# Optimization experiments

Measured on AMD Instinct MI355X. Metric: run time of the kernel, lower is better.

Reference implementation:

```python
import jax, jax.numpy as jnp
import numpy as np

B, S, H = 64, 512, 768
N_SPANS, MAX_SPAN, CW = 4, 8, 3
NH = 8
HD = H // NH
W = MAX_SPAN + 1 + 2 * CW  # max context window length (15)
H2 = H // 2
N_ATE, N_SENT = 2, 2


def _ln(x, g, b, eps=1e-5):
    m = x.mean(-1, keepdims=True)
    v = ((x - m) ** 2).mean(-1, keepdims=True)
    return (x - m) / jnp.sqrt(v + eps) * g + b


def _classifier(x, w1, b1, g, bb, w2, b2):
    # Dropout -> Linear -> GELU -> LayerNorm -> Linear (eval mode: dropout = id)
    h = jax.nn.gelu(x @ w1.T + b1, approximate=False)
    h = _ln(h, g, bb)
    return h @ w2.T + b2


def setup_inputs() -> dict:
    key = jax.random.key(0)
    ks = jax.random.split(key, 16)
    p = lambda k, shape: (0.02 * jax.random.normal(k, shape)).astype(jnp.float32)
    seq_out = jax.random.normal(ks[0], (B, S, H), dtype=jnp.float32)
    starts = jax.random.randint(ks[1], (B, N_SPANS), 1, S - MAX_SPAN - 1)
    lens = jax.random.randint(ks[2], (B, N_SPANS), 1, MAX_SPAN + 1)
    ends = starts + lens  # exclusive end, span length in [1, MAX_SPAN]
    return dict(
        seq_out=seq_out,
        span_starts=starts.astype(jnp.int32),
        span_ends=ends.astype(jnp.int32),
        ate_g=jnp.ones((H,), jnp.float32), ate_b=jnp.zeros((H,), jnp.float32),
        apc_g=jnp.ones((H,), jnp.float32), apc_b=jnp.zeros((H,), jnp.float32),
        w_in=p(ks[3], (3 * H, H)), b_in=jnp.zeros((3 * H,), jnp.float32),
        w_out=p(ks[4], (H, H)), b_out=jnp.zeros((H,), jnp.float32),
        fus_w=p(ks[5], (H, 2 * H)), fus_b=jnp.zeros((H,), jnp.float32),
        asp_w1=p(ks[6], (H2, H)), asp_b1=jnp.zeros((H2,), jnp.float32),
        asp_lng=jnp.ones((H2,), jnp.float32), asp_lnb=jnp.zeros((H2,), jnp.float32),
        asp_w2=p(ks[7], (N_ATE, H2)), asp_b2=jnp.zeros((N_ATE,), jnp.float32),
        sen_w1=p(ks[8], (H2, H)), sen_b1=jnp.zeros((H2,), jnp.float32),
        sen_lng=jnp.ones((H2,), jnp.float32), sen_lnb=jnp.zeros((H2,), jnp.float32),
        sen_w2=p(ks[9], (N_SENT, H2)), sen_b2=jnp.zeros((N_SENT,), jnp.float32),
    )


def _fwd(seq_out, ate_g, ate_b, apc_g, apc_b, w_in, b_in, w_out, b_out,
         fus_w, fus_b, asp_w1, asp_b1, asp_lng, asp_lnb, asp_w2, asp_b2,
         sen_w1, sen_b1, sen_lng, sen_lnb, sen_w2, sen_b2,
         span_starts, span_ends):
    dt = seq_out.dtype
    # clamping semantics as in the torch loop
    s = jnp.clip(span_starts, 0, S - 1)
    e = jnp.maximum(s, jnp.minimum(span_ends, S - 1))
    left = jnp.maximum(0, s - CW)
    right = jnp.minimum(S, e + 1 + CW)

    # ATE head over all tokens
    ate_logits = _classifier(_ln(seq_out, ate_g, ate_b),
                             asp_w1, asp_b1, asp_lng, asp_lnb, asp_w2, asp_b2)

    gather = jax.vmap(lambda so, idx: so[idx])  # ([S,H],[N,W]) -> [N,W,H]

    # aspect mean over tokens [s, e)
    aidx = s[..., None] + jnp.arange(MAX_SPAN)          # [B,N,MS]
    va = (aidx < e[..., None]).astype(dt)
    asp_tok = gather(seq_out, jnp.clip(aidx, 0, S - 1)) # [B,N,MS,H]
    cnt = va.sum(-1, keepdims=True)                     # [B,N,1]
    asp_mean = (asp_tok * va[..., None]).sum(-2) / jnp.maximum(cnt, 1.0)
    asp_mean = jnp.where(cnt > 0, asp_mean, seq_out[:, None, 0, :])

    # context window [left, right): tiny self-attention, then mean
    cidx = left[..., None] + jnp.arange(W)              # [B,N,W]
    vc = (cidx < right[..., None]).astype(dt)
    ctx = gather(seq_out, jnp.clip(cidx, 0, S - 1))     # [B,N,W,H]
    qkv = ctx @ w_in.T + b_in
    q, k, v = jnp.split(qkv, 3, axis=-1)
    q = q.reshape(B, N_SPANS, W, NH, HD) * (HD ** -0.5)
    k = k.reshape(B, N_SPANS, W, NH, HD)
    v = v.reshape(B, N_SPANS, W, NH, HD)
    scores = jnp.einsum('bnqhd,bnkhd->bnhqk', q, k)
    neg = jnp.asarray(jnp.finfo(dt).min, dt)
    scores = jnp.where(vc[:, :, None, None, :] > 0, scores, neg)
    attn = jax.nn.softmax(scores, axis=-1)
    out = jnp.einsum('bnhqk,bnkhd->bnqhd', attn, v).reshape(B, N_SPANS, W, H)
    out = out @ w_out.T + b_out
    ccnt = vc.sum(-1, keepdims=True)
    ctx_mean = (out * vc[..., None]).sum(-2) / jnp.maximum(ccnt, 1.0)

    combined = jnp.concatenate([asp_mean, ctx_mean], axis=-1)  # [B,N,2H]
    fused = jax.nn.gelu(combined @ fus_w.T + fus_b, approximate=False)
    apc_feat = fused.mean(axis=1)                              # [B,H]
    apc_logits = _classifier(_ln(apc_feat, apc_g, apc_b),
                             sen_w1, sen_b1, sen_lng, sen_lnb, sen_w2, sen_b2)
    return ate_logits, apc_logits


def reference(seq_out, span_starts, span_ends, ate_g, ate_b, apc_g, apc_b,
              w_in, b_in, w_out, b_out, fus_w, fus_b,
              asp_w1, asp_b1, asp_lng, asp_lnb, asp_w2, asp_b2,
              sen_w1, sen_b1, sen_lng, sen_lnb, sen_w2, sen_b2):
    return _fwd(seq_out, ate_g, ate_b, apc_g, apc_b, w_in, b_in, w_out, b_out,
                fus_w, fus_b, asp_w1, asp_b1, asp_lng, asp_lnb, asp_w2, asp_b2,
                sen_w1, sen_b1, sen_lng, sen_lnb, sen_w2, sen_b2,
                span_starts, span_ends)
```

## Files before the change

### kernel.cpp

```cpp
#include <hip/hip_runtime.h>
#include <math.h>

#define DEVI __device__ __forceinline__

using bf16x8 = __attribute__((ext_vector_type(8))) short;
using f32x4  = __attribute__((ext_vector_type(4))) float;

DEVI float b2f(unsigned short u) {
  union { unsigned int u; float f; } x; x.u = ((unsigned int)u) << 16; return x.f;
}
DEVI unsigned short f2b(float f) {
  union { float f; unsigned int u; } x; x.f = f;
  unsigned int r = (x.u + 0x7fffu + ((x.u >> 16) & 1u)) >> 16;
  return (unsigned short)r;
}
DEVI float gelu_f(float x) { return 0.5f * x * (1.0f + erff(x * 0.70710678118654752440f)); }

DEVI void wredxor2(float& a, float& b) {
  #pragma unroll
  for (int off = 32; off; off >>= 1) {
    a += __shfl_xor(a, off);
    b += __shfl_xor(b, off);
  }
}

template<int NW>
DEVI void breduce2(float& a, float& b) {
  __shared__ float buf[2 * NW];
  int lane = threadIdx.x & 63;
  int w = threadIdx.x >> 6;
  #pragma unroll
  for (int off = 32; off > 0; off >>= 1) {
    a += __shfl_down(a, off);
    b += __shfl_down(b, off);
  }
  if (lane == 0) { buf[w] = a; buf[NW + w] = b; }
  __syncthreads();
  float ra = 0.f, rb = 0.f;
  #pragma unroll
  for (int i = 0; i < NW; ++i) { ra += buf[i]; rb += buf[NW + i]; }
  a = ra; b = rb;
  __syncthreads();
}

DEVI void span_params(const int* st, const int* en, int span,
                      int& s, int& e, int& left, int& right) {
  int s0 = st[span], e0 = en[span];
  s = min(max(s0, 0), 511);
  e = max(s, min(e0, 511));
  left = max(0, s - 3);
  right = min(512, e + 4);
}

DEVI int xcd_logical(int bid, int n) {
  int q = n >> 3, r = n & 7;
  int xcd = bid & 7, idx = bid >> 3;
  return (xcd < r ? xcd * (q + 1) : r * (q + 1) + (xcd - r) * q) + idx;
}

__global__ __launch_bounds__(256) void prep_kernel(
    const float* __restrict__ w1, const float* __restrict__ w_in,
    const float* __restrict__ w_out, const float* __restrict__ fus_w,
    const float* __restrict__ sen_w1,
    unsigned short* __restrict__ d0, unsigned short* __restrict__ d1,
    unsigned short* __restrict__ d2, unsigned short* __restrict__ d3,
    unsigned short* __restrict__ d4,
    const float* __restrict__ seq, const float* __restrict__ ate_g,
    const float* __restrict__ ate_b, unsigned short* __restrict__ sbf,
    float2* __restrict__ stats, float2* __restrict__ c12,
    const int* __restrict__ st, const int* __restrict__ en,
    int* __restrict__ tokmap) {
  const int bid = blockIdx.x, tid = threadIdx.x;
  if (bid < 4032) {
    int i = bid * 256 + tid;
    if (i < 73728) {
      float4 v = reinterpret_cast<const float4*>(w1)[i];
      int k0 = (i * 4) % 768;
      float4 gv = *reinterpret_cast<const float4*>(ate_g + k0);
      ushort4 o;
      o.x = f2b(v.x * gv.x); o.y = f2b(v.y * gv.y);
      o.z = f2b(v.z * gv.z); o.w = f2b(v.w * gv.w);
      reinterpret_cast<ushort4*>(d0)[i] = o;
      return;
    }
    const float* s; unsigned short* d; int j;
    if (i < 516096)      { s = w_in;   d = d1; j = i - 73728; }
    else if (i < 663552) { s = w_out;  d = d2; j = i - 516096; }
    else if (i < 958464) { s = fus_w;  d = d3; j = i - 663552; }
    else                 { s = sen_w1; d = d4; j = i - 958464; }
    float4 v = reinterpret_cast<const float4*>(s)[j];
    ushort4 o;
    o.x = f2b(v.x); o.y = f2b(v.y); o.z = f2b(v.z); o.w = f2b(v.w);
    reinterpret_cast<ushort4*>(d)[j] = o;
  } else if (bid < 12224) {
    const int row = (bid - 4032) * 4 + (tid >> 6);
    const int lane = tid & 63;
    const float4* xr = reinterpret_cast<const float4*>(seq + (size_t)row * 768);
    float4 v[3];
    #pragma unroll
    for (int j = 0; j < 3; ++j) v[j] = xr[j * 64 + lane];
    float s = 0.f, q = 0.f;
    #pragma unroll
    for (int j = 0; j < 3; ++j) {
      s += v[j].x + v[j].y + v[j].z + v[j].w;
      q += v[j].x * v[j].x + v[j].y * v[j].y + v[j].z * v[j].z + v[j].w * v[j].w;
    }
    wredxor2(s, q);
    float mean = s * (1.0f / 768.0f);
    float rstd = rsqrtf(q * (1.0f / 768.0f) - mean * mean + 1e-5f);
    ushort4* orow = reinterpret_cast<ushort4*>(sbf + (size_t)row * 768);
    #pragma unroll
    for (int j = 0; j < 3; ++j) {
      ushort4 o;
      o.x = f2b(v[j].x); o.y = f2b(v[j].y); o.z = f2b(v[j].z); o.w = f2b(v[j].w);
      orow[j * 64 + lane] = o;
    }
    if (lane == 0) stats[row] = make_float2(rstd, rstd * mean);
  } else if (bid < 12320) {
    const int lane = tid & 63;
    const int j = (bid - 12224) * 4 + (tid >> 6);
    const float4* wr = reinterpret_cast<const float4*>(w1 + (size_t)j * 768);
    const float4* gp = reinterpret_cast<const float4*>(ate_g);
    const float4* bp = reinterpret_cast<const float4*>(ate_b);
    float a = 0.f, bsum = 0.f;
    #pragma unroll
    for (int i = 0; i < 3; ++i) {
      float4 wv = wr[i * 64 + lane];
      float4 gv = gp[i * 64 + lane];
      float4 bv = bp[i * 64 + lane];
      a    += gv.x * wv.x + gv.y * wv.y + gv.z * wv.z + gv.w * wv.w;
      bsum += bv.x * wv.x + bv.y * wv.y + bv.z * wv.z + bv.w * wv.w;
    }
    wredxor2(a, bsum);
    if (lane == 0) c12[j] = make_float2(a, bsum);
  } else {
    for (int i = tid; i < 3840; i += 256) {
      int span = i / 15, w = i % 15;
      int s, e, left, right;
      span_params(st, en, span, s, e, left, right);
      int b = span >> 2;
      tokmap[i] = b * 512 + min(left + w, 511);
    }
  }
}

template<int BM, int BN, int WM, int WN>
DEVI void gemm_core(const unsigned short* __restrict__ A,
                    const unsigned short* __restrict__ W,
                    int K, int bm, int bn,
                    unsigned short* As, unsigned short* Bs,
                    f32x4 (&acc)[WM / 16][WN / 16],
                    const int* __restrict__ rowmap = nullptr) {
  constexpr int CA = BM / 8;
  constexpr int CB = BN / 8;
  constexpr int NWC = BN / WN;
  constexpr int WAVES = (BM / WM) * NWC;
  constexpr int FM = WM / 16, FN = WN / 16;
  const int tid = threadIdx.x;
  const int lane = tid & 63;
  const int wv = tid >> 6;
  const int wr = wv / NWC, wc = wv % NWC;
  const int l16 = lane & 15, lhi = lane >> 4;
  const int srow = lane >> 3;
  const int scol = 8 * ((lane & 7) ^ srow);

  const int nt = K / 64;
  for (int t = 0; t < nt; ++t) {
    const int k0 = t * 64;
    #pragma unroll
    for (int ch = wv; ch < CA; ch += WAVES) {
      int ar = bm + ch * 8 + srow;
      size_t arow = rowmap ? (size_t)rowmap[ar] : (size_t)ar;
      __builtin_amdgcn_global_load_lds(
          (const __attribute__((address_space(1))) void*)&A[arow * K + k0 + scol],
          (__attribute__((address_space(3))) void*)&As[ch * 512], 16, 0, 0);
    }
    #pragma unroll
    for (int ch = wv; ch < CB; ch += WAVES)
      __builtin_amdgcn_global_load_lds(
          (const __attribute__((address_space(1))) void*)&W[(size_t)(bn + ch * 8 + srow) * K + k0 + scol],
          (__attribute__((address_space(3))) void*)&Bs[ch * 512], 16, 0, 0);
    __syncthreads();
    #pragma unroll
    for (int kk = 0; kk < 2; ++kk) {
      bf16x8 af[FM], bfr[FN];
      #pragma unroll
      for (int fm = 0; fm < FM; ++fm) {
        int r = wr * WM + fm * 16 + l16;
        af[fm] = *reinterpret_cast<const bf16x8*>(&As[r * 64 + ((kk * 32 + lhi * 8) ^ ((r & 7) * 8))]);
      }
      #pragma unroll
      for (int fn = 0; fn < FN; ++fn) {
        int r = wc * WN + fn * 16 + l16;
        bfr[fn] = *reinterpret_cast<const bf16x8*>(&Bs[r * 64 + ((kk * 32 + lhi * 8) ^ ((r & 7) * 8))]);
      }
      #pragma unroll
      for (int fm = 0; fm < FM; ++fm)
        #pragma unroll
        for (int fn = 0; fn < FN; ++fn)
          acc[fm][fn] = __builtin_amdgcn_mfma_f32_16x16x32_bf16(af[fm], bfr[fn], acc[fm][fn], 0, 0, 0);
    }
    __syncthreads();
  }
}

template<int BM, int BN, int WM, int WN>
DEVI void gemm_store(const float* __restrict__ bias, unsigned short* __restrict__ C,
                     int N, bool act, int bm, int bn, f32x4 (&acc)[WM / 16][WN / 16]) {
  constexpr int NWC = BN / WN;
  constexpr int FM = WM / 16, FN = WN / 16;
  const int lane = threadIdx.x & 63;
  const int wv = threadIdx.x >> 6;
  const int wr = wv / NWC, wc = wv % NWC;
  const int l16 = lane & 15, lhi = lane >> 4;
  #pragma unroll
  for (int fm = 0; fm < FM; ++fm) {
    #pragma unroll
    for (int fn = 0; fn < FN; ++fn) {
      int col = bn + wc * WN + fn * 16 + l16;
      float bv = bias[col];
      #pragma unroll
      for (int i = 0; i < 4; ++i) {
        int row = bm + wr * WM + fm * 16 + lhi * 4 + i;
        float v = acc[fm][fn][i] + bv;
        if (act) v = gelu_f(v);
        C[(size_t)row * N + col] = f2b(v);
      }
    }
  }
}

template<int BM, int BN, int WM, int WN, int ACT>
__global__ __launch_bounds__(256) void gemm_swz64(
    const unsigned short* __restrict__ A, const unsigned short* __restrict__ W,
    const float* __restrict__ bias, unsigned short* __restrict__ C,
    int M, int N, int K, int nbN) {
  __shared__ __align__(16) unsigned short As[BM * 64];
  __shared__ __align__(16) unsigned short Bs[BN * 64];
  int l = xcd_logical(blockIdx.x, gridDim.x);
  int mb = l / nbN, nb = l % nbN;
  f32x4 acc[WM / 16][WN / 16] = {};
  gemm_core<BM, BN, WM, WN>(A, W, K, mb * BM, nb * BN, As, Bs, acc);
  gemm_store<BM, BN, WM, WN>(bias, C, N, ACT != 0, mb * BM, nb * BN, acc);
}

__global__ __launch_bounds__(512) void dual_gemm_kernel(
    const unsigned short* __restrict__ sbf, const unsigned short* __restrict__ w1b,
    const float* __restrict__ b1, const float2* __restrict__ c12,
    const float2* __restrict__ stats, const float* __restrict__ lng,
    const float* __restrict__ w2, float4* __restrict__ hpart,
    const unsigned short* __restrict__ winb, const float* __restrict__ b_in,
    unsigned short* __restrict__ qkv, const int* __restrict__ tokmap) {
  __shared__ __align__(16) unsigned short lds[384 * 64];
  if (blockIdx.x < 384) {
    int l = xcd_logical(blockIdx.x, 384);
    int mb = l / 3, nb = l % 3;
    const int bm = mb * 256, bn = nb * 128;
    f32x4 acc[4][4] = {};
    gemm_core<256, 128, 64, 64>(sbf, w1b, 768, bm, bn, lds, lds + 256 * 64, acc);
    const int lane = threadIdx.x & 63;
    const int wv = threadIdx.x >> 6;
    const int wr = wv >> 1, wc = wv & 1;
    const int l16 = lane & 15, lhi = lane >> 4;
    float b1v[4], gw2a[4], gw2b[4], c1v[4], c2v[4];
    #pragma unroll
    for (int fn = 0; fn < 4; ++fn) {
      int col = bn + wc * 64 + fn * 16 + l16;
      b1v[fn] = b1[col];
      float2 cc = c12[col];
      c1v[fn] = cc.x; c2v[fn] = cc.y;
      float gg = lng[col];
      gw2a[fn] = gg * w2[col];
      gw2b[fn] = gg * w2[384 + col];
    }
    #pragma unroll
    for (int fm = 0; fm < 4; ++fm) {
      #pragma unroll
      for (int i = 0; i < 4; ++i) {
        int row = bm + wr * 64 + fm * 16 + lhi * 4 + i;
        float2 sr = stats[row];
        float s1 = 0.f, s2 = 0.f, q0 = 0.f, q1 = 0.f;
        #pragma unroll
        for (int fn = 0; fn < 4; ++fn) {
          float h = gelu_f(sr.x * acc[fm][fn][i] - sr.y * c1v[fn] + c2v[fn] + b1v[fn]);
          s1 += h; s2 += h * h;
          q0 += h * gw2a[fn]; q1 += h * gw2b[fn];
        }
        #pragma unroll
        for (int off = 1; off < 16; off <<= 1) {
          s1 += __shfl_xor(s1, off); s2 += __shfl_xor(s2, off);
          q0 += __shfl_xor(q0, off); q1 += __shfl_xor(q1, off);
        }
        if (l16 == 0) hpart[(size_t)row * 6 + nb * 2 + wc] = make_float4(s1, s2, q0, q1);
      }
    }
  } else {
    int bid = blockIdx.x - 384;
    int l = xcd_logical(bid, 270);
    int mb = l / 9, nb = l % 9;
    f32x4 acc[4][4] = {};
    gemm_core<128, 256, 64, 64>(sbf, winb, 768, mb * 128, nb * 256,
                                lds, lds + 128 * 64, acc, tokmap);
    gemm_store<128, 256, 64, 64>(b_in, qkv, 2304, false, mb * 128, nb * 256, acc);
  }
}

__global__ __launch_bounds__(256) void finattn_kernel(
    const float4* __restrict__ hpart, const float* __restrict__ lng,
    const float* __restrict__ lnb, const float* __restrict__ w2,
    const float* __restrict__ b2, float* __restrict__ out,
    const unsigned short* __restrict__ qkv, const int* __restrict__ st,
    const int* __restrict__ en, unsigned short* __restrict__ ctxO) {
  const int tid = threadIdx.x;
  if (blockIdx.x >= 2048) {
    __shared__ float cbuf[16];
    float c1a = 0.f, c1b = 0.f, c2a = 0.f, c2b = 0.f;
    for (int c = tid; c < 384; c += 256) {
      float gg = lng[c], bbv = lnb[c], wa = w2[c], wb = w2[384 + c];
      c1a += gg * wa; c1b += gg * wb;
      c2a += bbv * wa; c2b += bbv * wb;
    }
    wredxor2(c1a, c1b);
    wredxor2(c2a, c2b);
    if ((tid & 63) == 0) {
      int w = tid >> 6;
      cbuf[w * 4] = c1a; cbuf[w * 4 + 1] = c1b;
      cbuf[w * 4 + 2] = c2a; cbuf[w * 4 + 3] = c2b;
    }
    __syncthreads();
    c1a = cbuf[0] + cbuf[4] + cbuf[8] + cbuf[12];
    c1b = cbuf[1] + cbuf[5] + cbuf[9] + cbuf[13];
    c2a = cbuf[2] + cbuf[6] + cbuf[10] + cbuf[14];
    c2b = cbuf[3] + cbuf[7] + cbuf[11] + cbuf[15];
    const int row = (blockIdx.x - 2048) * 256 + tid;
    float S1 = 0.f, S2 = 0.f, D0 = 0.f, D1 = 0.f;
    #pragma unroll
    for (int p = 0; p < 6; ++p) {
      float4 v = hpart[(size_t)row * 6 + p];
      S1 += v.x; S2 += v.y; D0 += v.z; D1 += v.w;
    }
    float mu = S1 * (1.f / 384.f);
    float rstd = rsqrtf(S2 * (1.f / 384.f) - mu * mu + 1e-5f);
    out[(size_t)row * 2]     = rstd * (D0 - mu * c1a) + c2a + b2[0];
    out[(size_t)row * 2 + 1] = rstd * (D1 - mu * c1b) + c2b + b2[1];
    return;
  }
  __shared__ float qs[15][96], ks[15][96], vs[15][96];
  __shared__ float sc[15][16];
  const int span = blockIdx.x >> 3, hh = blockIdx.x & 7;
  int s, e, left, right;
  span_params(st, en, span, s, e, left, right);
  const int nv = right - left;
  const int r0 = span * 15;
  const float scale = 0.10206207261596576f;
  if (tid < 180) {
    int w = tid / 12, dp = tid % 12, d = dp * 8;
    const unsigned short* rowp = qkv + (size_t)(r0 + w) * 2304 + hh * 96 + d;
    bf16x8 qv = *reinterpret_cast<const bf16x8*>(rowp);
    bf16x8 kv = *reinterpret_cast<const bf16x8*>(rowp + 768);
    bf16x8 vv = *reinterpret_cast<const bf16x8*>(rowp + 1536);
    #pragma unroll
    for (int j = 0; j < 8; ++j) {
      qs[w][d + j] = b2f((unsigned short)qv[j]) * scale;
      ks[w][d + j] = b2f((unsigned short)kv[j]);
      vs[w][d + j] = b2f((unsigned short)vv[j]);
    }
  }
  __syncthreads();
  if (tid < 225) {
    int i = tid / 15, j = tid % 15;
    float a = 0.f;
    #pragma unroll
    for (int d = 0; d < 96; ++d) a += qs[i][d] * ks[j][d];
    sc[i][j] = (j < nv) ? a : -3.402823466e38f;
  }
  __syncthreads();
  if (tid < 15) {
    int i = tid;
    float m = -3.402823466e38f;
    #pragma unroll
    for (int j = 0; j < 15; ++j) m = fmaxf(m, sc[i][j]);
    float ex[15];
    float ssum = 0.f;
    #pragma unroll
    for (int j = 0; j < 15; ++j) { ex[j] = expf(sc[i][j] - m); ssum += ex[j]; }
    float inv = 1.0f / ssum;
    #pragma unroll
    for (int j = 0; j < 15; ++j) sc[i][j] = ex[j] * inv;
  }
  __syncthreads();
  for (int idx = tid; idx < 720; idx += 256) {
    int w = idx / 48, dp = idx % 48, d = dp * 2;
    float o0 = 0.f, o1 = 0.f;
    #pragma unroll
    for (int j = 0; j < 15; ++j) {
      float p = sc[w][j];
      o0 += p * vs[j][d];
      o1 += p * vs[j][d + 1];
    }
    ushort2 o; o.x = f2b(o0); o.y = f2b(o1);
    *reinterpret_cast<ushort2*>(&ctxO[(size_t)(r0 + w) * 768 + hh * 96 + d]) = o;
  }
}

__global__ __launch_bounds__(256) void means_kernel(
    const unsigned short* __restrict__ sbf, const unsigned short* __restrict__ projO,
    const int* __restrict__ st, const int* __restrict__ en,
    unsigned short* __restrict__ comb) {
  const int span = blockIdx.x;
  int s, e, left, right;
  span_params(st, en, span, s, e, left, right);
  int b = span >> 2;
  int e2 = min(e, s + 8);
  int cnt = e2 - s;
  int nv = right - left;
  float inva = (cnt > 0) ? 1.0f / (float)cnt : 0.f;
  float invc = 1.0f / (float)nv;
  for (int c = threadIdx.x; c < 768; c += 256) {
    float sa = 0.f;
    for (int t = s; t < e2; ++t) sa += b2f(sbf[((size_t)b * 512 + t) * 768 + c]);
    float asp = (cnt > 0) ? sa * inva : b2f(sbf[((size_t)b * 512) * 768 + c]);
    comb[(size_t)span * 1536 + c] = f2b(asp);
    float sc_ = 0.f;
    for (int w = 0; w < nv; ++w) sc_ += b2f(projO[(size_t)(span * 15 + w) * 768 + c]);
    comb[(size_t)span * 1536 + 768 + c] = f2b(sc_ * invc);
  }
}

__global__ __launch_bounds__(256) void apc_all_kernel(
    const unsigned short* __restrict__ fused, const float* __restrict__ g,
    const float* __restrict__ bb, const unsigned short* __restrict__ senb,
    const float* __restrict__ b1, const float* __restrict__ lng,
    const float* __restrict__ lnb, const float* __restrict__ w2,
    const float* __restrict__ b2, float* __restrict__ out) {
  const int b = blockIdx.x, tid = threadIdx.x;
  __shared__ float xs[768];
  __shared__ float hs[384];
  float v[3];
  #pragma unroll
  for (int j = 0; j < 3; ++j) {
    int c = tid + j * 256;
    float a = 0.f;
    #pragma unroll
    for (int n = 0; n < 4; ++n) a += b2f(fused[((size_t)(b * 4 + n)) * 768 + c]);
    v[j] = 0.25f * a;
  }
  float s = v[0] + v[1] + v[2];
  float q = v[0] * v[0] + v[1] * v[1] + v[2] * v[2];
  breduce2<4>(s, q);
  float mean = s * (1.f / 768.f);
  float rstd = rsqrtf(q * (1.f / 768.f) - mean * mean + 1e-5f);
  #pragma unroll
  for (int j = 0; j < 3; ++j) {
    int c = tid + j * 256;
    xs[c] = (v[j] - mean) * rstd * g[c] + bb[c];
  }
  __syncthreads();
  for (int j = tid; j < 384; j += 256) {
    const bf16x8* wrp = reinterpret_cast<const bf16x8*>(senb + (size_t)j * 768);
    float dot = 0.f;
    #pragma unroll 4
    for (int k8 = 0; k8 < 96; ++k8) {
      bf16x8 wv = wrp[k8];
      #pragma unroll
      for (int u = 0; u < 8; ++u) dot += xs[k8 * 8 + u] * b2f((unsigned short)wv[u]);
    }
    hs[j] = gelu_f(dot + b1[j]);
  }
  __syncthreads();
  s = 0.f; q = 0.f;
  for (int j = tid; j < 384; j += 256) { float h = hs[j]; s += h; q += h * h; }
  breduce2<4>(s, q);
  mean = s * (1.f / 384.f);
  rstd = rsqrtf(q * (1.f / 384.f) - mean * mean + 1e-5f);
  float p0 = 0.f, p1 = 0.f;
  for (int j = tid; j < 384; j += 256) {
    float hl = (hs[j] - mean) * rstd * lng[j] + lnb[j];
    p0 += hl * w2[j];
    p1 += hl * w2[384 + j];
  }
  breduce2<4>(p0, p1);
  if (tid == 0) {
    out[b * 2]     = p0 + b2[0];
    out[b * 2 + 1] = p1 + b2[1];
  }
}

extern "C" void kernel_launch(void* const* d_in, const int* in_sizes, int n_in,
                              void* d_out, int out_size, void* d_ws, size_t ws_size,
                              hipStream_t stream) {
  const float* seq    = (const float*)d_in[0];
  const int*   st     = (const int*)d_in[1];
  const int*   en     = (const int*)d_in[2];
  const float* ate_g  = (const float*)d_in[3];
  const float* ate_b  = (const float*)d_in[4];
  const float* apc_g  = (const float*)d_in[5];
  const float* apc_b  = (const float*)d_in[6];
  const float* w_in   = (const float*)d_in[7];
  const float* b_in   = (const float*)d_in[8];
  const float* w_out  = (const float*)d_in[9];
  const float* b_out  = (const float*)d_in[10];
  const float* fus_w  = (const float*)d_in[11];
  const float* fus_b  = (const float*)d_in[12];
  const float* asp_w1 = (const float*)d_in[13];
  const float* asp_b1 = (const float*)d_in[14];
  const float* asp_lng= (const float*)d_in[15];
  const float* asp_lnb= (const float*)d_in[16];
  const float* asp_w2 = (const float*)d_in[17];
  const float* asp_b2 = (const float*)d_in[18];
  const float* sen_w1 = (const float*)d_in[19];
  const float* sen_b1 = (const float*)d_in[20];
  const float* sen_lng= (const float*)d_in[21];
  const float* sen_lnb= (const float*)d_in[22];
  const float* sen_w2 = (const float*)d_in[23];
  const float* sen_b2 = (const float*)d_in[24];
  float* out = (float*)d_out;

  char* wsb = (char*)d_ws;
  unsigned short* sbf   = (unsigned short*)(wsb + 0);
  float2*        stats  = (float2*)(wsb + 50331648);
  float2*        c12    = (float2*)(wsb + 50593792);
  int*           tokmap = (int*)(wsb + 50596864);
  unsigned short* qkvb  = (unsigned short*)(wsb + 50612224);
  unsigned short* ctxO  = (unsigned short*)(wsb + 68306944);
  unsigned short* projO = (unsigned short*)(wsb + 74205184);
  unsigned short* comb  = (unsigned short*)(wsb + 80103424);
  unsigned short* fusO  = (unsigned short*)(wsb + 80889856);
  float4*        hpart  = (float4*)(wsb + 81283072);
  const size_t off_w = 84428800;
  unsigned short* w1b   = (unsigned short*)(wsb + off_w);
  unsigned short* winb  = (unsigned short*)(wsb + off_w + 589824);
  unsigned short* woutb = (unsigned short*)(wsb + off_w + 4128768);
  unsigned short* fusb  = (unsigned short*)(wsb + off_w + 5308416);
  unsigned short* senb  = (unsigned short*)(wsb + off_w + 7667712);

  prep_kernel<<<12321, 256, 0, stream>>>(asp_w1, w_in, w_out, fus_w, sen_w1,
                                         w1b, winb, woutb, fusb, senb,
                                         seq, ate_g, ate_b, sbf, stats, c12,
                                         st, en, tokmap);
  dual_gemm_kernel<<<654, 512, 0, stream>>>(sbf, w1b, asp_b1, c12, stats,
                                            asp_lng, asp_w2, hpart,
                                            winb, b_in, qkvb, tokmap);
  finattn_kernel<<<2176, 256, 0, stream>>>(hpart, asp_lng, asp_lnb, asp_w2, asp_b2, out,
                                           qkvb, st, en, ctxO);
  gemm_swz64<64, 128, 32, 64, 0><<<360, 256, 0, stream>>>(
      ctxO, woutb, b_out, projO, 3840, 768, 768, 6);
  means_kernel<<<256, 256, 0, stream>>>(sbf, projO, st, en, comb);
  gemm_swz64<64, 64, 32, 32, 1><<<48, 256, 0, stream>>>(
      comb, fusb, fus_b, fusO, 256, 768, 1536, 12);
  apc_all_kernel<<<64, 256, 0, stream>>>(fusO, apc_g, apc_b, senb, sen_b1,
                                         sen_lng, sen_lnb, sen_w2, sen_b2, out + 65536);
}
```

Before: 184.9 us.

## Average attention context before output projection, shrinking out-proj GEMM to span rows

Uses linearity of the output projection: the masked mean over context positions is taken on the attention output first (via summed softmax weights times V), and then a single 256-row GEMM with w_out is applied, writing directly into the second half of the concatenated buffer. This removes the 3840-row out-projection GEMM, the per-position ctxO writes and the separate means kernel, whose aspect-mean part moves into extra blocks of the attention kernel. The GEMM core also precomputes per-thread global load offsets outside the k-loop. Rounding now happens at different points (bf16 averaged context), so numerics shift slightly.

```diff
diff --git a/kernel.cpp b/kernel.cpp
--- a/kernel.cpp
+++ b/kernel.cpp
@@ -155,6 +155,8 @@
   constexpr int CB = BN / 8;
   constexpr int NWC = BN / WN;
   constexpr int WAVES = (BM / WM) * NWC;
+  constexpr int CPA = CA / WAVES;
+  constexpr int CPB = CB / WAVES;
   constexpr int FM = WM / 16, FN = WN / 16;
   const int tid = threadIdx.x;
   const int lane = tid & 63;
@@ -164,22 +166,29 @@
   const int srow = lane >> 3;
   const int scol = 8 * ((lane & 7) ^ srow);
 
+  size_t aoff[CPA], boff[CPB];
+  #pragma unroll
+  for (int c = 0; c < CPA; ++c) {
+    int ar = bm + (wv + c * WAVES) * 8 + srow;
+    aoff[c] = (rowmap ? (size_t)rowmap[ar] : (size_t)ar) * K + scol;
+  }
+  #pragma unroll
+  for (int c = 0; c < CPB; ++c)
+    boff[c] = (size_t)(bn + (wv + c * WAVES) * 8 + srow) * K + scol;
+
   const int nt = K / 64;
   for (int t = 0; t < nt; ++t) {
     const int k0 = t * 64;
     #pragma unroll
-    for (int ch = wv; ch < CA; ch += WAVES) {
-      int ar = bm + ch * 8 + srow;
-      size_t arow = rowmap ? (size_t)rowmap[ar] : (size_t)ar;
+    for (int c = 0; c < CPA; ++c)
       __builtin_amdgcn_global_load_lds(
-          (const __attribute__((address_space(1))) void*)&A[arow * K + k0 + scol],
-          (__attribute__((address_space(3))) void*)&As[ch * 512], 16, 0, 0);
-    }
-    #pragma unroll
-    for (int ch = wv; ch < CB; ch += WAVES)
+          (const __attribute__((address_space(1))) void*)&A[aoff[c] + k0],
+          (__attribute__((address_space(3))) void*)&As[(wv + c * WAVES) * 512], 16, 0, 0);
+    #pragma unroll
+    for (int c = 0; c < CPB; ++c)
       __builtin_amdgcn_global_load_lds(
-          (const __attribute__((address_space(1))) void*)&W[(size_t)(bn + ch * 8 + srow) * K + k0 + scol],
-          (__attribute__((address_space(3))) void*)&Bs[ch * 512], 16, 0, 0);
+          (const __attribute__((address_space(1))) void*)&W[boff[c] + k0],
+          (__attribute__((address_space(3))) void*)&Bs[(wv + c * WAVES) * 512], 16, 0, 0);
     __syncthreads();
     #pragma unroll
     for (int kk = 0; kk < 2; ++kk) {
@@ -206,7 +215,7 @@
 
 template<int BM, int BN, int WM, int WN>
 DEVI void gemm_store(const float* __restrict__ bias, unsigned short* __restrict__ C,
-                     int N, bool act, int bm, int bn, f32x4 (&acc)[WM / 16][WN / 16]) {
+                     int NSTRIDE, bool act, int bm, int bn, f32x4 (&acc)[WM / 16][WN / 16]) {
   constexpr int NWC = BN / WN;
   constexpr int FM = WM / 16, FN = WN / 16;
   const int lane = threadIdx.x & 63;
@@ -224,7 +233,7 @@
         int row = bm + wr * WM + fm * 16 + lhi * 4 + i;
         float v = acc[fm][fn][i] + bv;
         if (act) v = gelu_f(v);
-        C[(size_t)row * N + col] = f2b(v);
+        C[(size_t)row * NSTRIDE + col] = f2b(v);
       }
     }
   }
@@ -234,14 +243,14 @@
 __global__ __launch_bounds__(256) void gemm_swz64(
     const unsigned short* __restrict__ A, const unsigned short* __restrict__ W,
     const float* __restrict__ bias, unsigned short* __restrict__ C,
-    int M, int N, int K, int nbN) {
+    int M, int NSTRIDE, int K, int nbN) {
   __shared__ __align__(16) unsigned short As[BM * 64];
   __shared__ __align__(16) unsigned short Bs[BN * 64];
   int l = xcd_logical(blockIdx.x, gridDim.x);
   int mb = l / nbN, nb = l % nbN;
   f32x4 acc[WM / 16][WN / 16] = {};
   gemm_core<BM, BN, WM, WN>(A, W, K, mb * BM, nb * BN, As, Bs, acc);
-  gemm_store<BM, BN, WM, WN>(bias, C, N, ACT != 0, mb * BM, nb * BN, acc);
+  gemm_store<BM, BN, WM, WN>(bias, C, NSTRIDE, ACT != 0, mb * BM, nb * BN, acc);
 }
 
 __global__ __launch_bounds__(512) void dual_gemm_kernel(
@@ -310,8 +319,25 @@
     const float* __restrict__ lnb, const float* __restrict__ w2,
     const float* __restrict__ b2, float* __restrict__ out,
     const unsigned short* __restrict__ qkv, const int* __restrict__ st,
-    const int* __restrict__ en, unsigned short* __restrict__ ctxO) {
+    const int* __restrict__ en, unsigned short* __restrict__ cavg,
+    const unsigned short* __restrict__ sbf, unsigned short* __restrict__ comb) {
   const int tid = threadIdx.x;
+  if (blockIdx.x >= 2176) {
+    const int span = blockIdx.x - 2176;
+    int s, e, left, right;
+    span_params(st, en, span, s, e, left, right);
+    int b = span >> 2;
+    int e2 = min(e, s + 8);
+    int cnt = e2 - s;
+    float inva = (cnt > 0) ? 1.0f / (float)cnt : 0.f;
+    for (int c = tid; c < 768; c += 256) {
+      float sa = 0.f;
+      for (int t = s; t < e2; ++t) sa += b2f(sbf[((size_t)b * 512 + t) * 768 + c]);
+      float asp = (cnt > 0) ? sa * inva : b2f(sbf[((size_t)b * 512) * 768 + c]);
+      comb[(size_t)span * 1536 + c] = f2b(asp);
+    }
+    return;
+  }
   if (blockIdx.x >= 2048) {
     __shared__ float cbuf[16];
     float c1a = 0.f, c1b = 0.f, c2a = 0.f, c2b = 0.f;
@@ -347,6 +373,7 @@
   }
   __shared__ float qs[15][96], ks[15][96], vs[15][96];
   __shared__ float sc[15][16];
+  __shared__ float wsum[15];
   const int span = blockIdx.x >> 3, hh = blockIdx.x & 7;
   int s, e, left, right;
   span_params(st, en, span, s, e, left, right);
@@ -389,41 +416,19 @@
     for (int j = 0; j < 15; ++j) sc[i][j] = ex[j] * inv;
   }
   __syncthreads();
-  for (int idx = tid; idx < 720; idx += 256) {
-    int w = idx / 48, dp = idx % 48, d = dp * 2;
-    float o0 = 0.f, o1 = 0.f;
-    #pragma unroll
-    for (int j = 0; j < 15; ++j) {
-      float p = sc[w][j];
-      o0 += p * vs[j][d];
-      o1 += p * vs[j][d + 1];
-    }
-    ushort2 o; o.x = f2b(o0); o.y = f2b(o1);
-    *reinterpret_cast<ushort2*>(&ctxO[(size_t)(r0 + w) * 768 + hh * 96 + d]) = o;
-  }
-}
-
-__global__ __launch_bounds__(256) void means_kernel(
-    const unsigned short* __restrict__ sbf, const unsigned short* __restrict__ projO,
-    const int* __restrict__ st, const int* __restrict__ en,
-    unsigned short* __restrict__ comb) {
-  const int span = blockIdx.x;
-  int s, e, left, right;
-  span_params(st, en, span, s, e, left, right);
-  int b = span >> 2;
-  int e2 = min(e, s + 8);
-  int cnt = e2 - s;
-  int nv = right - left;
-  float inva = (cnt > 0) ? 1.0f / (float)cnt : 0.f;
-  float invc = 1.0f / (float)nv;
-  for (int c = threadIdx.x; c < 768; c += 256) {
-    float sa = 0.f;
-    for (int t = s; t < e2; ++t) sa += b2f(sbf[((size_t)b * 512 + t) * 768 + c]);
-    float asp = (cnt > 0) ? sa * inva : b2f(sbf[((size_t)b * 512) * 768 + c]);
-    comb[(size_t)span * 1536 + c] = f2b(asp);
-    float sc_ = 0.f;
-    for (int w = 0; w < nv; ++w) sc_ += b2f(projO[(size_t)(span * 15 + w) * 768 + c]);
-    comb[(size_t)span * 1536 + 768 + c] = f2b(sc_ * invc);
+  if (tid < 15) {
+    int j = tid;
+    float a = 0.f;
+    for (int i = 0; i < nv; ++i) a += sc[i][j];
+    wsum[j] = a;
+  }
+  __syncthreads();
+  if (tid < 96) {
+    int d = tid;
+    float r = 0.f;
+    #pragma unroll
+    for (int j = 0; j < 15; ++j) r += wsum[j] * vs[j][d];
+    cavg[(size_t)span * 768 + hh * 96 + d] = f2b(r / (float)nv);
   }
 }
 
@@ -522,12 +527,11 @@
   float2*        c12    = (float2*)(wsb + 50593792);
   int*           tokmap = (int*)(wsb + 50596864);
   unsigned short* qkvb  = (unsigned short*)(wsb + 50612224);
-  unsigned short* ctxO  = (unsigned short*)(wsb + 68306944);
-  unsigned short* projO = (unsigned short*)(wsb + 74205184);
-  unsigned short* comb  = (unsigned short*)(wsb + 80103424);
-  unsigned short* fusO  = (unsigned short*)(wsb + 80889856);
-  float4*        hpart  = (float4*)(wsb + 81283072);
-  const size_t off_w = 84428800;
+  unsigned short* cavg  = (unsigned short*)(wsb + 68306944);
+  unsigned short* comb  = (unsigned short*)(wsb + 68700160);
+  unsigned short* fusO  = (unsigned short*)(wsb + 69486592);
+  float4*        hpart  = (float4*)(wsb + 69879808);
+  const size_t off_w = 73025536;
   unsigned short* w1b   = (unsigned short*)(wsb + off_w);
   unsigned short* winb  = (unsigned short*)(wsb + off_w + 589824);
   unsigned short* woutb = (unsigned short*)(wsb + off_w + 4128768);
@@ -541,11 +545,10 @@
   dual_gemm_kernel<<<654, 512, 0, stream>>>(sbf, w1b, asp_b1, c12, stats,
                                             asp_lng, asp_w2, hpart,
                                             winb, b_in, qkvb, tokmap);
-  finattn_kernel<<<2176, 256, 0, stream>>>(hpart, asp_lng, asp_lnb, asp_w2, asp_b2, out,
-                                           qkvb, st, en, ctxO);
-  gemm_swz64<64, 128, 32, 64, 0><<<360, 256, 0, stream>>>(
-      ctxO, woutb, b_out, projO, 3840, 768, 768, 6);
-  means_kernel<<<256, 256, 0, stream>>>(sbf, projO, st, en, comb);
+  finattn_kernel<<<2432, 256, 0, stream>>>(hpart, asp_lng, asp_lnb, asp_w2, asp_b2, out,
+                                           qkvb, st, en, cavg, sbf, comb);
+  gemm_swz64<64, 128, 32, 64, 0><<<24, 256, 0, stream>>>(
+      cavg, woutb, b_out, comb + 768, 256, 1536, 768, 6);
   gemm_swz64<64, 64, 32, 32, 1><<<48, 256, 0, stream>>>(
       comb, fusb, fus_b, fusO, 256, 768, 1536, 12);
   apc_all_kernel<<<64, 256, 0, stream>>>(fusO, apc_g, apc_b, senb, sen_b1,
```

After: 161.7 us. -12.5%, faster.
